# Optimization experiments

Hardware: AMD Instinct MI355X
Metric: run time of the kernel (lower is better)

The kernel has to match this reference:

```python
import jax, jax.numpy as jnp
import numpy as np

HEADS = 16
DIM_HEAD = 64
SCALE = DIM_HEAD ** -0.5
LN_EPS = 1e-5


def setup_inputs() -> dict:
    key = jax.random.key(0)
    k1, k2, k3 = jax.random.split(key, 3)
    b, s, d = 2, 2048, 1024
    inner = HEADS * DIM_HEAD
    x = jax.random.normal(k1, (b, s, d), dtype=jnp.float32)
    w_qkv = jax.random.normal(k2, (d, 3 * inner), dtype=jnp.float32) * (d ** -0.5)
    w_out = jax.random.normal(k3, (inner, d), dtype=jnp.float32) * (inner ** -0.5)
    return {
        "x": x,
        "ln_gamma": jnp.ones((d,), jnp.float32),
        "ln_beta": jnp.zeros((d,), jnp.float32),
        "w_qkv": w_qkv,
        "w_out": w_out,
        "b_out": jnp.zeros((d,), jnp.float32),
    }


def _layernorm(x, gamma, beta):
    mu = jnp.mean(x, axis=-1, keepdims=True)
    var = jnp.var(x, axis=-1, keepdims=True)
    return (x - mu) * jax.lax.rsqrt(var + LN_EPS) * gamma + beta


def reference(x, ln_gamma, ln_beta, w_qkv, w_out, b_out):
    b, s, d = x.shape
    xn = _layernorm(x, ln_gamma, ln_beta)
    qkv = xn @ w_qkv                       # [b, s, 3*inner]
    q, k, v = jnp.split(qkv, 3, axis=-1)
    def heads(t):
        return t.reshape(b, s, HEADS, DIM_HEAD).transpose(0, 2, 1, 3)  # [b, h, s, dh]
    q, k, v = heads(q), heads(k), heads(v)
    dots = jnp.einsum("bhqd,bhkd->bhqk", q, k) * SCALE   # [b, h, s, s]
    attn = jax.nn.softmax(dots, axis=-1)
    out = jnp.einsum("bhqk,bhkd->bhqd", attn, v)          # [b, h, s, dh]
    out = out.transpose(0, 2, 1, 3).reshape(b, s, HEADS * DIM_HEAD)
    return out @ w_out + b_out
```

## Files before the change

### kernel.cpp

```cpp
#include <hip/hip_runtime.h>
#include <hip/hip_bf16.h>
#include <stdint.h>

#define NH     16
#define DHEAD  64
#define SEQ    2048
#define DMODEL 1024
#define NBATCH 2
#define INNER  1024
#define QKVN   3072
#define ROWS   4096
#define ATT_QB 128
#define ATT_KB 64
#define KSPLIT 2

typedef __attribute__((ext_vector_type(8))) __bf16 bf16x8;
typedef __attribute__((ext_vector_type(4))) float floatx4;

__device__ __forceinline__ unsigned short f2bf(float f) {
    union { __bf16 b; unsigned short u; } c; c.b = (__bf16)f; return c.u;
}

typedef __attribute__((address_space(1))) void gvoid;
typedef __attribute__((address_space(3))) void lvoid;
__device__ __forceinline__ void gl_lds16(const void* g, void* l) {
    __builtin_amdgcn_global_load_lds((gvoid*)g, (lvoid*)l, 16, 0, 0);
}

__global__ __launch_bounds__(256) void transpose_f2b(
        const float* __restrict__ in, unsigned short* __restrict__ out,
        int rows, int cols) {
    __shared__ unsigned short tile[32][33];
    const int bx = blockIdx.x * 32, by = blockIdx.y * 32;
    const int tx = threadIdx.x & 31, ty = threadIdx.x >> 5;
    for (int i = ty; i < 32; i += 8)
        tile[i][tx] = f2bf(in[(size_t)(by + i) * cols + bx + tx]);
    __syncthreads();
    for (int i = ty; i < 32; i += 8)
        out[(size_t)(bx + i) * rows + by + tx] = tile[tx][i];
}

__global__ __launch_bounds__(256) void ln_kernel(
        const float* __restrict__ x,
        const float* __restrict__ gamma,
        const float* __restrict__ beta,
        unsigned short* __restrict__ xn) {
    __shared__ float red[4][2];
    const int row = blockIdx.x, t = threadIdx.x;
    const size_t base = (size_t)row * DMODEL + t * 4;
    float4 v = *(const float4*)(x + base);
    float s  = v.x + v.y + v.z + v.w;
    float ss = v.x*v.x + v.y*v.y + v.z*v.z + v.w*v.w;
    for (int off = 32; off >= 1; off >>= 1) {
        s  += __shfl_xor(s,  off);
        ss += __shfl_xor(ss, off);
    }
    const int w = t >> 6, lane = t & 63;
    if (lane == 0) { red[w][0] = s; red[w][1] = ss; }
    __syncthreads();
    if (t == 0) {
        float S  = red[0][0] + red[1][0] + red[2][0] + red[3][0];
        float SS = red[0][1] + red[1][1] + red[2][1] + red[3][1];
        float mu  = S * (1.f / DMODEL);
        float var = SS * (1.f / DMODEL) - mu * mu;
        red[0][0] = mu; red[0][1] = rsqrtf(var + 1e-5f);
    }
    __syncthreads();
    const float mu = red[0][0], rstd = red[0][1];
    float4 g = *(const float4*)(gamma + t * 4);
    float4 bb = *(const float4*)(beta + t * 4);
    ushort4 o;
    o.x = f2bf((v.x - mu) * rstd * g.x + bb.x);
    o.y = f2bf((v.y - mu) * rstd * g.y + bb.y);
    o.z = f2bf((v.z - mu) * rstd * g.z + bb.z);
    o.w = f2bf((v.w - mu) * rstd * g.w + bb.w);
    *(ushort4*)(xn + base) = o;
}

__global__ __launch_bounds__(256) void gemm_qkv(
        const unsigned short* __restrict__ A,
        const unsigned short* __restrict__ Bt,
        unsigned short* __restrict__ qP,
        unsigned short* __restrict__ kP,
        unsigned short* __restrict__ vT) {
    const int K = DMODEL;
    __shared__ __align__(16) unsigned short sA[128 * 32];
    __shared__ __align__(16) unsigned short sB[128 * 32];
    __shared__ __align__(16) unsigned short tb[2][64 * 72];
    const int t = threadIdx.x;
    const int mBase = blockIdx.y * 128, nBase = blockIdx.x * 128;
    const int w = t >> 6, lane = t & 63, quad = lane >> 4, l16 = lane & 15;
    const int wm = (w >> 1) * 64, wn = (w & 1) * 64;
    const int srow = t >> 2, sch = t & 3;
    floatx4 acc[4][4];
    for (int mi = 0; mi < 4; mi++)
        for (int ni = 0; ni < 4; ni++) acc[mi][ni] = (floatx4)0.f;

    for (int k0 = 0; k0 < K; k0 += 32) {
        #pragma unroll
        for (int c = 0; c < 2; c++) {
            const int row = c * 64 + srow;
            const int gcol = (sch ^ ((row >> 1) & 3)) * 8;
            gl_lds16(&A[(size_t)(mBase + row) * K + k0 + gcol], &sA[(c * 256 + w * 64) * 8]);
            gl_lds16(&Bt[(size_t)(nBase + row) * K + k0 + gcol], &sB[(c * 256 + w * 64) * 8]);
        }
        __syncthreads();
        bf16x8 af[4], bfv[4];
        #pragma unroll
        for (int mi = 0; mi < 4; mi++) {
            const int r = wm + mi * 16 + l16;
            af[mi] = *(const bf16x8*)&sA[r * 32 + (quad ^ ((r >> 1) & 3)) * 8];
        }
        #pragma unroll
        for (int ni = 0; ni < 4; ni++) {
            const int r = wn + ni * 16 + l16;
            bfv[ni] = *(const bf16x8*)&sB[r * 32 + (quad ^ ((r >> 1) & 3)) * 8];
        }
        #pragma unroll
        for (int mi = 0; mi < 4; mi++)
            #pragma unroll
            for (int ni = 0; ni < 4; ni++)
                acc[mi][ni] = __builtin_amdgcn_mfma_f32_16x16x32_bf16(
                    af[mi], bfv[ni], acc[mi][ni], 0, 0, 0);
        __syncthreads();
    }
    const int reg = nBase >> 10;
    if (reg == 2) {
        #pragma unroll
        for (int ni = 0; ni < 4; ni++) {
            const int col = nBase + wn + ni * 16 + l16;
            const int h = (col & 1023) >> 6, dh = col & 63;
            #pragma unroll
            for (int mi = 0; mi < 4; mi++) {
                const int row0 = mBase + wm + mi * 16 + quad * 4;
                const int b = row0 >> 11, s0 = row0 & 2047;
                ushort4 o;
                o.x = f2bf(acc[mi][ni][0]); o.y = f2bf(acc[mi][ni][1]);
                o.z = f2bf(acc[mi][ni][2]); o.w = f2bf(acc[mi][ni][3]);
                *(ushort4*)&vT[((size_t)(b * NH + h) * DHEAD + dh) * SEQ + s0] = o;
            }
        }
    } else {
        unsigned short* dst = (reg == 0) ? qP : kP;
        const float scl = (reg == 0) ? 0.125f : 1.f;
        const int hh = ((nBase + wn) & 1023) >> 6;
        #pragma unroll
        for (int ph = 0; ph < 2; ph++) {
            if ((w >> 1) == ph) {
                unsigned short* tb_ = &tb[w & 1][0];
                #pragma unroll
                for (int mi = 0; mi < 4; mi++)
                    #pragma unroll
                    for (int ni = 0; ni < 4; ni++)
                        #pragma unroll
                        for (int i = 0; i < 4; i++)
                            tb_[(mi * 16 + quad * 4 + i) * 72 + ni * 16 + l16] =
                                f2bf(acc[mi][ni][i] * scl);
                asm volatile("s_waitcnt lgkmcnt(0)" ::: "memory");
                const int row_g = mBase + wm + lane;
                const int b = row_g >> 11, sr = row_g & 2047;
                unsigned short* orow = dst + ((size_t)(b * NH + hh) * SEQ + sr) * DHEAD;
                #pragma unroll
                for (int c = 0; c < 8; c++)
                    *(bf16x8*)&orow[c * 8] = *(const bf16x8*)&tb_[lane * 72 + c * 8];
            }
            __syncthreads();
        }
    }
}

__global__ __launch_bounds__(256) void gemm_out(
        const unsigned short* __restrict__ A,
        const unsigned short* __restrict__ Bt,
        float* __restrict__ C,
        const int M, const int N, const int K,
        const float* __restrict__ bias) {
    __shared__ __align__(16) unsigned short sA[128 * 32];
    __shared__ __align__(16) unsigned short sB[64 * 32];
    const int t = threadIdx.x;
    const int mBase = blockIdx.y * 128, nBase = blockIdx.x * 64;
    const int w = t >> 6, lane = t & 63, quad = lane >> 4, l16 = lane & 15;
    const int wm = (w >> 1) * 64, wn = (w & 1) * 32;
    const int srow = t >> 2, sch = t & 3;
    floatx4 acc[4][2];
    for (int mi = 0; mi < 4; mi++)
        for (int ni = 0; ni < 2; ni++) acc[mi][ni] = (floatx4)0.f;

    for (int k0 = 0; k0 < K; k0 += 32) {
        #pragma unroll
        for (int c = 0; c < 2; c++) {
            const int row = c * 64 + srow;
            const int gcol = (sch ^ ((row >> 1) & 3)) * 8;
            gl_lds16(&A[(size_t)(mBase + row) * K + k0 + gcol], &sA[(c * 256 + w * 64) * 8]);
        }
        {
            const int gcol = (sch ^ ((srow >> 1) & 3)) * 8;
            gl_lds16(&Bt[(size_t)(nBase + srow) * K + k0 + gcol], &sB[(w * 64) * 8]);
        }
        __syncthreads();
        bf16x8 af[4], bfv[2];
        #pragma unroll
        for (int mi = 0; mi < 4; mi++) {
            const int r = wm + mi * 16 + l16;
            af[mi] = *(const bf16x8*)&sA[r * 32 + (quad ^ ((r >> 1) & 3)) * 8];
        }
        #pragma unroll
        for (int ni = 0; ni < 2; ni++) {
            const int r = wn + ni * 16 + l16;
            bfv[ni] = *(const bf16x8*)&sB[r * 32 + (quad ^ ((r >> 1) & 3)) * 8];
        }
        #pragma unroll
        for (int mi = 0; mi < 4; mi++)
            #pragma unroll
            for (int ni = 0; ni < 2; ni++)
                acc[mi][ni] = __builtin_amdgcn_mfma_f32_16x16x32_bf16(
                    af[mi], bfv[ni], acc[mi][ni], 0, 0, 0);
        __syncthreads();
    }
    #pragma unroll
    for (int mi = 0; mi < 4; mi++)
        #pragma unroll
        for (int ni = 0; ni < 2; ni++) {
            const int col = nBase + wn + ni * 16 + l16;
            const float badd = bias ? bias[col] : 0.f;
            #pragma unroll
            for (int i = 0; i < 4; i++) {
                const int row = mBase + wm + mi * 16 + quad * 4 + i;
                C[(size_t)row * N + col] = acc[mi][ni][i] + badd;
            }
        }
}

__global__ __launch_bounds__(256) void attn_kernel(
        const unsigned short* __restrict__ qP,
        const unsigned short* __restrict__ kP,
        const unsigned short* __restrict__ vT,
        float* __restrict__ Opart,
        float* __restrict__ lpart) {
    __shared__ __align__(16) unsigned short sK[2][ATT_KB * 64];
    __shared__ __align__(16) unsigned short sV[2][ATT_KB * 64];
    __shared__ __align__(16) unsigned short sP[4][2][16 * 64];
    const int t = threadIdx.x, w = t >> 6, lane = t & 63;
    const int quad = lane >> 4, l16 = lane & 15;
    const int bh = blockIdx.y, b = bh >> 4, h = bh & 15;
    const int z = blockIdx.z;
    const int kvBase = z * (SEQ / KSPLIT);
    const int qbase = blockIdx.x * ATT_QB + w * 32;
    const int swr = l16 & 7;

    bf16x8 aq[2][2];
    #pragma unroll
    for (int st = 0; st < 2; st++)
        #pragma unroll
        for (int hh = 0; hh < 2; hh++)
            aq[st][hh] = *(const bf16x8*)&qP[
                ((size_t)bh * SEQ + qbase + st * 16 + l16) * DHEAD + hh * 32 + quad * 8];

    floatx4 oac[2][4];
    float lS[2] = {0.f, 0.f};
    #pragma unroll
    for (int st = 0; st < 2; st++)
        #pragma unroll
        for (int c = 0; c < 4; c++) oac[st][c] = (floatx4)0.f;

    const unsigned short* kb = kP + (size_t)bh * SEQ * DHEAD;
    const unsigned short* vb = vT + (size_t)bh * DHEAD * SEQ;
    const int r8 = lane >> 3, sw8 = ((lane & 7) ^ r8) * 8;

    auto stage = [&](int it, int bi) {
        const int kv0 = kvBase + it * ATT_KB;
        #pragma unroll
        for (int ii = 0; ii < 2; ii++) {
            const int row = w * 16 + ii * 8 + r8;
            gl_lds16(kb + (size_t)(kv0 + row) * DHEAD + sw8,
                     (void*)&sK[bi][(w * 16 + ii * 8) * 64]);
            gl_lds16(vb + (size_t)row * SEQ + kv0 + sw8,
                     (void*)&sV[bi][(w * 16 + ii * 8) * 64]);
        }
    };
    stage(0, 0);

    const int NIT = SEQ / KSPLIT / ATT_KB;
    for (int it = 0; it < NIT; ++it) {
        __syncthreads();
        if (it + 1 < NIT) stage(it + 1, (it + 1) & 1);
        const unsigned short* sKb = &sK[it & 1][0];
        const unsigned short* sVb = &sV[it & 1][0];

        bf16x8 kf[4][2];
        #pragma unroll
        for (int c = 0; c < 4; c++)
            #pragma unroll
            for (int hh = 0; hh < 2; hh++)
                kf[c][hh] = *(const bf16x8*)&sKb[(c * 16 + l16) * 64 +
                                                 8 * (((hh << 2) | quad) ^ swr)];
        floatx4 sv[2][4];
        #pragma unroll
        for (int st = 0; st < 2; st++)
            #pragma unroll
            for (int c = 0; c < 4; c++) {
                floatx4 a = (floatx4)0.f;
                a = __builtin_amdgcn_mfma_f32_16x16x32_bf16(kf[c][0], aq[st][0], a, 0, 0, 0);
                a = __builtin_amdgcn_mfma_f32_16x16x32_bf16(kf[c][1], aq[st][1], a, 0, 0, 0);
                sv[st][c] = a;
            }
        #pragma unroll
        for (int st = 0; st < 2; st++) {
            float sum = 0.f;
            unsigned short* pb = (unsigned short*)&sP[w][st][0];
            #pragma unroll
            for (int c = 0; c < 4; c++) {
                float p0 = __expf(sv[st][c][0]), p1 = __expf(sv[st][c][1]);
                float p2 = __expf(sv[st][c][2]), p3 = __expf(sv[st][c][3]);
                sum += (p0 + p1) + (p2 + p3);
                ushort4 pk;
                pk.x = f2bf(p0); pk.y = f2bf(p1); pk.z = f2bf(p2); pk.w = f2bf(p3);
                *(ushort4*)&pb[l16 * 64 + 8 * ((((c << 1) | (quad >> 1))) ^ swr) + (quad & 1) * 4] = pk;
            }
            sum += __shfl_xor(sum, 16);
            sum += __shfl_xor(sum, 32);
            lS[st] += sum;
        }
        bf16x8 vf[4][2];
        #pragma unroll
        for (int c = 0; c < 4; c++)
            #pragma unroll
            for (int hh = 0; hh < 2; hh++)
                vf[c][hh] = *(const bf16x8*)&sVb[(c * 16 + l16) * 64 +
                                                 8 * (((hh << 2) | quad) ^ swr)];
        asm volatile("s_waitcnt lgkmcnt(0)" ::: "memory");
        #pragma unroll
        for (int st = 0; st < 2; st++) {
            const unsigned short* pb = (const unsigned short*)&sP[w][st][0];
            bf16x8 pf[2];
            #pragma unroll
            for (int hh = 0; hh < 2; hh++)
                pf[hh] = *(const bf16x8*)&pb[l16 * 64 + 8 * (((hh << 2) | quad) ^ swr)];
            #pragma unroll
            for (int c = 0; c < 4; c++) {
                oac[st][c] = __builtin_amdgcn_mfma_f32_16x16x32_bf16(vf[c][0], pf[0], oac[st][c], 0, 0, 0);
                oac[st][c] = __builtin_amdgcn_mfma_f32_16x16x32_bf16(vf[c][1], pf[1], oac[st][c], 0, 0, 0);
            }
        }
    }
    float* Ob = Opart + (size_t)z * ROWS * INNER;
    #pragma unroll
    for (int st = 0; st < 2; st++) {
        const size_t rb = (size_t)(b * SEQ + qbase + st * 16 + l16) * INNER + h * DHEAD;
        #pragma unroll
        for (int c = 0; c < 4; c++) {
            float4 o;
            o.x = oac[st][c][0]; o.y = oac[st][c][1];
            o.z = oac[st][c][2]; o.w = oac[st][c][3];
            *(float4*)&Ob[rb + c * 16 + quad * 4] = o;
        }
    }
    if (quad == 0) {
        #pragma unroll
        for (int st = 0; st < 2; st++)
            lpart[((size_t)z * NBATCH * NH + bh) * SEQ + qbase + st * 16 + l16] = lS[st];
    }
}

__global__ __launch_bounds__(256) void attn_combine(
        const float* __restrict__ Opart,
        const float* __restrict__ lpart,
        unsigned short* __restrict__ aout) {
    const int row = blockIdx.x, t = threadIdx.x;
    const int b = row >> 11, s = row & 2047;
    __shared__ float rls[16];
    if (t < 16) {
        const size_t i0 = ((size_t)(b * NH + t)) * SEQ + s;
        rls[t] = 1.f / (lpart[i0] + lpart[(size_t)NBATCH * NH * SEQ + i0]);
    }
    __syncthreads();
    const size_t base = (size_t)row * INNER + t * 4;
    float4 o0 = *(const float4*)(Opart + base);
    float4 o1 = *(const float4*)(Opart + (size_t)ROWS * INNER + base);
    const float rl = rls[t >> 4];
    ushort4 o;
    o.x = f2bf((o0.x + o1.x) * rl);
    o.y = f2bf((o0.y + o1.y) * rl);
    o.z = f2bf((o0.z + o1.z) * rl);
    o.w = f2bf((o0.w + o1.w) * rl);
    *(ushort4*)&aout[base] = o;
}

extern "C" void kernel_launch(void* const* d_in, const int* in_sizes, int n_in,
                              void* d_out, int out_size, void* d_ws, size_t ws_size,
                              hipStream_t stream) {
    const float* x     = (const float*)d_in[0];
    const float* gamma = (const float*)d_in[1];
    const float* beta  = (const float*)d_in[2];
    const float* wqkv  = (const float*)d_in[3];
    const float* wout  = (const float*)d_in[4];
    const float* bout  = (const float*)d_in[5];
    float* out = (float*)d_out;

    unsigned short* ws     = (unsigned short*)d_ws;
    unsigned short* xn     = ws;
    unsigned short* wqkvT  = xn     + (size_t)ROWS * DMODEL;
    unsigned short* qPb    = wqkvT  + (size_t)QKVN * DMODEL;
    unsigned short* kPb    = qPb    + (size_t)NBATCH * NH * SEQ * DHEAD;
    unsigned short* vTb    = kPb    + (size_t)NBATCH * NH * SEQ * DHEAD;
    unsigned short* attnO  = vTb    + (size_t)NBATCH * NH * SEQ * DHEAD;
    unsigned short* woutT  = attnO  + (size_t)ROWS * INNER;
    float* Opart = (float*)(woutT + (size_t)DMODEL * INNER);
    float* lpart = Opart + (size_t)KSPLIT * ROWS * INNER;

    transpose_f2b<<<dim3(QKVN / 32, DMODEL / 32), 256, 0, stream>>>(wqkv, wqkvT, DMODEL, QKVN);
    transpose_f2b<<<dim3(DMODEL / 32, INNER / 32), 256, 0, stream>>>(wout, woutT, INNER, DMODEL);
    ln_kernel<<<ROWS, 256, 0, stream>>>(x, gamma, beta, xn);
    gemm_qkv<<<dim3(QKVN / 128, ROWS / 128), 256, 0, stream>>>(xn, wqkvT, qPb, kPb, vTb);
    attn_kernel<<<dim3(SEQ / ATT_QB, NBATCH * NH, KSPLIT), 256, 0, stream>>>(
        qPb, kPb, vTb, Opart, lpart);
    attn_combine<<<ROWS, 256, 0, stream>>>(Opart, lpart, attnO);
    gemm_out<<<dim3(DMODEL / 64, ROWS / 128), 256, 0, stream>>>(
        attnO, woutT, out, ROWS, DMODEL, INNER, bout);
}
```

Before: 226.2 us.

## Drop KV split and combine kernel; smaller Q tiles, XCD-aware mapping, exp2

Removes the two-way KV split and the separate combine kernel. Each block now handles 64 queries (16 per wave) over the full sequence and writes normalized bf16 output directly, which avoids the fp32 partial-output round trip through memory. Blocks are remapped so each XCD handles a contiguous set of heads, improving L2 reuse of K/V. The Q scale folds in log2(e) so the kernel can use hardware exp2, and s_setprio is raised around the MFMA sections. This trades fewer MFMAs per K/V load (K/V are re-read by twice as many blocks) for less global traffic and one fewer launch.

```diff
diff --git a/kernel.cpp b/kernel.cpp
--- a/kernel.cpp
+++ b/kernel.cpp
@@ -10,15 +10,22 @@
 #define INNER  1024
 #define QKVN   3072
 #define ROWS   4096
-#define ATT_QB 128
+#define ATT_QB 64
 #define ATT_KB 64
-#define KSPLIT 2
 
 typedef __attribute__((ext_vector_type(8))) __bf16 bf16x8;
 typedef __attribute__((ext_vector_type(4))) float floatx4;
 
 __device__ __forceinline__ unsigned short f2bf(float f) {
     union { __bf16 b; unsigned short u; } c; c.b = (__bf16)f; return c.u;
+}
+
+__device__ __forceinline__ float fexp2(float x) {
+#if __has_builtin(__builtin_amdgcn_exp2f)
+    return __builtin_amdgcn_exp2f(x);
+#else
+    float r; asm("v_exp_f32 %0, %1" : "=v"(r) : "v"(x)); return r;
+#endif
 }
 
 typedef __attribute__((address_space(1))) void gvoid;
@@ -142,7 +149,7 @@
         }
     } else {
         unsigned short* dst = (reg == 0) ? qP : kP;
-        const float scl = (reg == 0) ? 0.125f : 1.f;
+        const float scl = (reg == 0) ? 0.18033688011112042f : 1.f;
         const int hh = ((nBase + wn) & 1023) >> 6;
         #pragma unroll
         for (int ph = 0; ph < 2; ph++) {
@@ -231,44 +238,41 @@
         }
 }
 
-__global__ __launch_bounds__(256) void attn_kernel(
+__global__ __launch_bounds__(256, 4) void attn_kernel(
         const unsigned short* __restrict__ qP,
         const unsigned short* __restrict__ kP,
         const unsigned short* __restrict__ vT,
-        float* __restrict__ Opart,
-        float* __restrict__ lpart) {
+        unsigned short* __restrict__ aout) {
     __shared__ __align__(16) unsigned short sK[2][ATT_KB * 64];
     __shared__ __align__(16) unsigned short sV[2][ATT_KB * 64];
-    __shared__ __align__(16) unsigned short sP[4][2][16 * 64];
+    __shared__ __align__(16) unsigned short sP[4][16 * 64];
     const int t = threadIdx.x, w = t >> 6, lane = t & 63;
     const int quad = lane >> 4, l16 = lane & 15;
-    const int bh = blockIdx.y, b = bh >> 4, h = bh & 15;
-    const int z = blockIdx.z;
-    const int kvBase = z * (SEQ / KSPLIT);
-    const int qbase = blockIdx.x * ATT_QB + w * 32;
+    const int bid = blockIdx.x;
+    const int xcd = bid & 7, slot = bid >> 3;
+    const int bh = xcd * 4 + (slot >> 5);
+    const int qb = slot & 31;
+    const int b = bh >> 4, h = bh & 15;
+    const int qbase = qb * ATT_QB + w * 16;
     const int swr = l16 & 7;
 
-    bf16x8 aq[2][2];
+    bf16x8 aq[2];
     #pragma unroll
-    for (int st = 0; st < 2; st++)
-        #pragma unroll
-        for (int hh = 0; hh < 2; hh++)
-            aq[st][hh] = *(const bf16x8*)&qP[
-                ((size_t)bh * SEQ + qbase + st * 16 + l16) * DHEAD + hh * 32 + quad * 8];
-
-    floatx4 oac[2][4];
-    float lS[2] = {0.f, 0.f};
+    for (int hh = 0; hh < 2; hh++)
+        aq[hh] = *(const bf16x8*)&qP[
+            ((size_t)bh * SEQ + qbase + l16) * DHEAD + hh * 32 + quad * 8];
+
+    floatx4 oac[4];
+    float lS = 0.f;
     #pragma unroll
-    for (int st = 0; st < 2; st++)
-        #pragma unroll
-        for (int c = 0; c < 4; c++) oac[st][c] = (floatx4)0.f;
+    for (int c = 0; c < 4; c++) oac[c] = (floatx4)0.f;
 
     const unsigned short* kb = kP + (size_t)bh * SEQ * DHEAD;
     const unsigned short* vb = vT + (size_t)bh * DHEAD * SEQ;
     const int r8 = lane >> 3, sw8 = ((lane & 7) ^ r8) * 8;
 
     auto stage = [&](int it, int bi) {
-        const int kv0 = kvBase + it * ATT_KB;
+        const int kv0 = it * ATT_KB;
         #pragma unroll
         for (int ii = 0; ii < 2; ii++) {
             const int row = w * 16 + ii * 8 + r8;
@@ -280,7 +284,7 @@
     };
     stage(0, 0);
 
-    const int NIT = SEQ / KSPLIT / ATT_KB;
+    const int NIT = SEQ / ATT_KB;
     for (int it = 0; it < NIT; ++it) {
         __syncthreads();
         if (it + 1 < NIT) stage(it + 1, (it + 1) & 1);
@@ -294,24 +298,23 @@
             for (int hh = 0; hh < 2; hh++)
                 kf[c][hh] = *(const bf16x8*)&sKb[(c * 16 + l16) * 64 +
                                                  8 * (((hh << 2) | quad) ^ swr)];
-        floatx4 sv[2][4];
-        #pragma unroll
-        for (int st = 0; st < 2; st++)
+        floatx4 sv[4];
+        __builtin_amdgcn_s_setprio(1);
+        #pragma unroll
+        for (int c = 0; c < 4; c++) {
+            floatx4 a = (floatx4)0.f;
+            a = __builtin_amdgcn_mfma_f32_16x16x32_bf16(kf[c][0], aq[0], a, 0, 0, 0);
+            a = __builtin_amdgcn_mfma_f32_16x16x32_bf16(kf[c][1], aq[1], a, 0, 0, 0);
+            sv[c] = a;
+        }
+        __builtin_amdgcn_s_setprio(0);
+        {
+            float sum = 0.f;
+            unsigned short* pb = (unsigned short*)&sP[w][0];
             #pragma unroll
             for (int c = 0; c < 4; c++) {
-                floatx4 a = (floatx4)0.f;
-                a = __builtin_amdgcn_mfma_f32_16x16x32_bf16(kf[c][0], aq[st][0], a, 0, 0, 0);
-                a = __builtin_amdgcn_mfma_f32_16x16x32_bf16(kf[c][1], aq[st][1], a, 0, 0, 0);
-                sv[st][c] = a;
-            }
-        #pragma unroll
-        for (int st = 0; st < 2; st++) {
-            float sum = 0.f;
-            unsigned short* pb = (unsigned short*)&sP[w][st][0];
-            #pragma unroll
-            for (int c = 0; c < 4; c++) {
-                float p0 = __expf(sv[st][c][0]), p1 = __expf(sv[st][c][1]);
-                float p2 = __expf(sv[st][c][2]), p3 = __expf(sv[st][c][3]);
+                float p0 = fexp2(sv[c][0]), p1 = fexp2(sv[c][1]);
+                float p2 = fexp2(sv[c][2]), p3 = fexp2(sv[c][3]);
                 sum += (p0 + p1) + (p2 + p3);
                 ushort4 pk;
                 pk.x = f2bf(p0); pk.y = f2bf(p1); pk.z = f2bf(p2); pk.w = f2bf(p3);
@@ -319,7 +322,7 @@
             }
             sum += __shfl_xor(sum, 16);
             sum += __shfl_xor(sum, 32);
-            lS[st] += sum;
+            lS += sum;
         }
         bf16x8 vf[4][2];
         #pragma unroll
@@ -329,61 +332,32 @@
                 vf[c][hh] = *(const bf16x8*)&sVb[(c * 16 + l16) * 64 +
                                                  8 * (((hh << 2) | quad) ^ swr)];
         asm volatile("s_waitcnt lgkmcnt(0)" ::: "memory");
-        #pragma unroll
-        for (int st = 0; st < 2; st++) {
-            const unsigned short* pb = (const unsigned short*)&sP[w][st][0];
+        {
+            const unsigned short* pb = (const unsigned short*)&sP[w][0];
             bf16x8 pf[2];
             #pragma unroll
             for (int hh = 0; hh < 2; hh++)
                 pf[hh] = *(const bf16x8*)&pb[l16 * 64 + 8 * (((hh << 2) | quad) ^ swr)];
+            __builtin_amdgcn_s_setprio(1);
             #pragma unroll
             for (int c = 0; c < 4; c++) {
-                oac[st][c] = __builtin_amdgcn_mfma_f32_16x16x32_bf16(vf[c][0], pf[0], oac[st][c], 0, 0, 0);
-                oac[st][c] = __builtin_amdgcn_mfma_f32_16x16x32_bf16(vf[c][1], pf[1], oac[st][c], 0, 0, 0);
-            }
-        }
-    }
-    float* Ob = Opart + (size_t)z * ROWS * INNER;
+                oac[c] = __builtin_amdgcn_mfma_f32_16x16x32_bf16(vf[c][0], pf[0], oac[c], 0, 0, 0);
+                oac[c] = __builtin_amdgcn_mfma_f32_16x16x32_bf16(vf[c][1], pf[1], oac[c], 0, 0, 0);
+            }
+            __builtin_amdgcn_s_setprio(0);
+        }
+    }
+    const float rl = 1.f / lS;
+    unsigned short* orow = aout + ((size_t)(b * SEQ + qbase + l16)) * INNER + h * DHEAD;
     #pragma unroll
-    for (int st = 0; st < 2; st++) {
-        const size_t rb = (size_t)(b * SEQ + qbase + st * 16 + l16) * INNER + h * DHEAD;
-        #pragma unroll
-        for (int c = 0; c < 4; c++) {
-            float4 o;
-            o.x = oac[st][c][0]; o.y = oac[st][c][1];
-            o.z = oac[st][c][2]; o.w = oac[st][c][3];
-            *(float4*)&Ob[rb + c * 16 + quad * 4] = o;
-        }
-    }
-    if (quad == 0) {
-        #pragma unroll
-        for (int st = 0; st < 2; st++)
-            lpart[((size_t)z * NBATCH * NH + bh) * SEQ + qbase + st * 16 + l16] = lS[st];
-    }
-}
-
-__global__ __launch_bounds__(256) void attn_combine(
-        const float* __restrict__ Opart,
-        const float* __restrict__ lpart,
-        unsigned short* __restrict__ aout) {
-    const int row = blockIdx.x, t = threadIdx.x;
-    const int b = row >> 11, s = row & 2047;
-    __shared__ float rls[16];
-    if (t < 16) {
-        const size_t i0 = ((size_t)(b * NH + t)) * SEQ + s;
-        rls[t] = 1.f / (lpart[i0] + lpart[(size_t)NBATCH * NH * SEQ + i0]);
-    }
-    __syncthreads();
-    const size_t base = (size_t)row * INNER + t * 4;
-    float4 o0 = *(const float4*)(Opart + base);
-    float4 o1 = *(const float4*)(Opart + (size_t)ROWS * INNER + base);
-    const float rl = rls[t >> 4];
-    ushort4 o;
-    o.x = f2bf((o0.x + o1.x) * rl);
-    o.y = f2bf((o0.y + o1.y) * rl);
-    o.z = f2bf((o0.z + o1.z) * rl);
-    o.w = f2bf((o0.w + o1.w) * rl);
-    *(ushort4*)&aout[base] = o;
+    for (int c = 0; c < 4; c++) {
+        ushort4 o;
+        o.x = f2bf(oac[c][0] * rl);
+        o.y = f2bf(oac[c][1] * rl);
+        o.z = f2bf(oac[c][2] * rl);
+        o.w = f2bf(oac[c][3] * rl);
+        *(ushort4*)&orow[c * 16 + quad * 4] = o;
+    }
 }
 
 extern "C" void kernel_launch(void* const* d_in, const int* in_sizes, int n_in,
@@ -405,16 +379,13 @@
     unsigned short* vTb    = kPb    + (size_t)NBATCH * NH * SEQ * DHEAD;
     unsigned short* attnO  = vTb    + (size_t)NBATCH * NH * SEQ * DHEAD;
     unsigned short* woutT  = attnO  + (size_t)ROWS * INNER;
-    float* Opart = (float*)(woutT + (size_t)DMODEL * INNER);
-    float* lpart = Opart + (size_t)KSPLIT * ROWS * INNER;
 
     transpose_f2b<<<dim3(QKVN / 32, DMODEL / 32), 256, 0, stream>>>(wqkv, wqkvT, DMODEL, QKVN);
     transpose_f2b<<<dim3(DMODEL / 32, INNER / 32), 256, 0, stream>>>(wout, woutT, INNER, DMODEL);
     ln_kernel<<<ROWS, 256, 0, stream>>>(x, gamma, beta, xn);
     gemm_qkv<<<dim3(QKVN / 128, ROWS / 128), 256, 0, stream>>>(xn, wqkvT, qPb, kPb, vTb);
-    attn_kernel<<<dim3(SEQ / ATT_QB, NBATCH * NH, KSPLIT), 256, 0, stream>>>(
-        qPb, kPb, vTb, Opart, lpart);
-    attn_combine<<<ROWS, 256, 0, stream>>>(Opart, lpart, attnO);
+    attn_kernel<<<dim3((SEQ / ATT_QB) * NBATCH * NH), 256, 0, stream>>>(
+        qPb, kPb, vTb, attnO);
     gemm_out<<<dim3(DMODEL / 64, ROWS / 128), 256, 0, stream>>>(
         attnO, woutT, out, ROWS, DMODEL, INNER, bout);
 }
```

Result: faster. 216.4 us (-4.3%).
